# Performance work log

Hardware: AMD Instinct MI355X
Metric: run time of the kernel (lower is better)

## Reference

```python
import jax, jax.numpy as jnp
import numpy as np


def setup_inputs() -> dict:
    key = jax.random.key(0)
    k1, k2, k3, k4 = jax.random.split(key, 4)
    B, IN, OUT, R = 4096, 4096, 4096, 256
    x = jax.random.normal(k1, (B, IN), dtype=jnp.float32)
    U = jax.random.normal(k2, (R, IN), dtype=jnp.float32) / np.sqrt(IN)
    V = jax.random.normal(k3, (OUT, R), dtype=jnp.float32) / np.sqrt(R)
    bias = jax.random.uniform(k4, (OUT,), dtype=jnp.float32,
                              minval=-IN ** -0.5, maxval=IN ** -0.5)
    return {"x": x, "U": U, "V": V, "bias": bias}


def reference(x, U, V, bias):
    # Low-rank linear: out[b,j] = sum_k V[j,k] * (sum_i U[k,i] * x[b,i]) + bias[j]
    # (the torch loops with sparsity=1.0 / keep_stride==1 compute exactly this)
    t = jnp.einsum('bi,ri->br', x, U)        # [B, R]
    out = jnp.einsum('br,or->bo', t, V) + bias  # [B, OUT]
    return out
```

## Files before the change

### kernel.cpp

```cpp
#include <hip/hip_runtime.h>

typedef __attribute__((ext_vector_type(8))) short bf16x8;
typedef __attribute__((ext_vector_type(4))) float f32x4;

__device__ __forceinline__ unsigned short f2bf(float f) {
  unsigned int u = __float_as_uint(f);
  return (unsigned short)((u + 0x7fffu + ((u >> 16) & 1u)) >> 16);
}

__device__ __forceinline__ float bf2f(unsigned short s) {
  return __uint_as_float(((unsigned int)s) << 16);
}

__device__ __forceinline__ void gload_lds16(const void* g, void* l) {
  __builtin_amdgcn_global_load_lds((const __attribute__((address_space(1))) void*)g,
                                   (__attribute__((address_space(3))) void*)l,
                                   16, 0, 0);
}

__global__ void prep(const float* __restrict__ U, const float4* __restrict__ V,
                     unsigned short* __restrict__ Upk, ushort4* __restrict__ Vb) {
  int i = blockIdx.x * 256 + threadIdx.x;
  const int NUP = 128 * 16 * 64;
  if (i < NUP) {
    int l = i & 63, n = (i >> 6) & 15, jg = i >> 10;
    const float* src = U + (long long)(n * 16 + (l & 15)) * 4096 + jg * 32 + (l >> 4) * 8;
    float4 a = *(const float4*)src;
    float4 b = *(const float4*)(src + 4);
    ushort4 o0, o1;
    o0.x = f2bf(a.x); o0.y = f2bf(a.y); o0.z = f2bf(a.z); o0.w = f2bf(a.w);
    o1.x = f2bf(b.x); o1.y = f2bf(b.y); o1.z = f2bf(b.z); o1.w = f2bf(b.w);
    ushort4* d = (ushort4*)(Upk + (long long)i * 8);
    d[0] = o0; d[1] = o1;
  } else {
    int j = i - NUP;
    float4 v = V[j];
    ushort4 o;
    o.x = f2bf(v.x); o.y = f2bf(v.y); o.z = f2bf(v.z); o.w = f2bf(v.w);
    Vb[j] = o;
  }
}

__global__ __launch_bounds__(256, 1)
void gemm1_ures(const float* __restrict__ x, const unsigned short* __restrict__ Upk,
                unsigned short* __restrict__ P) {
  __shared__ unsigned short sU[8 * 16 * 64 * 8];

  const int tid = threadIdx.x;
  const int l = tid & 63;
  const int w = tid >> 6;
  const int mg = blockIdx.x;
  const int z  = blockIdx.z;
  const int lr = l & 15;
  const int lg = l >> 4;

  {
    const unsigned short* src = Upk + (long long)z * 65536;
#pragma unroll
    for (int is = 0; is < 32; ++is) {
      int eo = is * 2048 + tid * 8;
      gload_lds16(src + eo, &sU[eo]);
    }
  }

  const float* xbase = x + (long long)(mg * 256 + w * 16 + lr) * 4096 + z * 256 + lg * 8;

  float4 xr[2][8][2];
#define XLOAD(p, s)                                                     \
  {                                                                     \
    const float* px_ = xbase + (long long)(p) * 64 * 4096;              \
    _Pragma("unroll")                                                   \
    for (int j_ = 0; j_ < 8; ++j_) {                                    \
      xr[s][j_][0] = *(const float4*)(px_ + j_ * 32);                   \
      xr[s][j_][1] = *(const float4*)(px_ + j_ * 32 + 4);               \
    }                                                                   \
  }

  XLOAD(0, 0);
  __syncthreads();

  unsigned short* Pz = P + (long long)z * (4096LL * 256);

#pragma unroll
  for (int p = 0; p < 4; ++p) {
    if (p < 3) XLOAD(p + 1, (p + 1) & 1);
    f32x4 acc[16] = {};
#pragma unroll
    for (int j = 0; j < 8; ++j) {
      float4 u0 = xr[p & 1][j][0], u1 = xr[p & 1][j][1];
      bf16x8 af;
      af[0] = (short)f2bf(u0.x); af[1] = (short)f2bf(u0.y);
      af[2] = (short)f2bf(u0.z); af[3] = (short)f2bf(u0.w);
      af[4] = (short)f2bf(u1.x); af[5] = (short)f2bf(u1.y);
      af[6] = (short)f2bf(u1.z); af[7] = (short)f2bf(u1.w);
#pragma unroll
      for (int n = 0; n < 16; ++n) {
        bf16x8 bfr = *(const bf16x8*)&sU[((j * 16 + n) * 64 + l) * 8];
        acc[n] = __builtin_amdgcn_mfma_f32_16x16x32_bf16(af, bfr, acc[n], 0, 0, 0);
      }
    }
    const int r0 = mg * 256 + p * 64 + w * 16 + lg * 4;
#pragma unroll
    for (int n = 0; n < 16; ++n)
#pragma unroll
      for (int i2 = 0; i2 < 4; ++i2)
        Pz[(long long)(r0 + i2) * 256 + n * 16 + lr] = f2bf(acc[n][i2]);
  }
#undef XLOAD
}

__global__ void reduce16(const ushort4* __restrict__ P, ushort4* __restrict__ t) {
  const int S = 4096 * 256 / 4;
  int i = blockIdx.x * 256 + threadIdx.x;
  float sx = 0, sy = 0, sz = 0, sw = 0;
#pragma unroll
  for (int z = 0; z < 16; ++z) {
    ushort4 v = P[i + z * S];
    sx += bf2f(v.x); sy += bf2f(v.y); sz += bf2f(v.z); sw += bf2f(v.w);
  }
  ushort4 o;
  o.x = f2bf(sx); o.y = f2bf(sy); o.z = f2bf(sz); o.w = f2bf(sw);
  t[i] = o;
}

__global__ __launch_bounds__(256)
void gemm2(const unsigned short* __restrict__ A,
           const unsigned short* __restrict__ B,
           const float* __restrict__ bias,
           float* __restrict__ C) {
  constexpr int MREP = 4, NREP = 4;
  __shared__ unsigned short sA[2][128 * 32];
  __shared__ unsigned short sB[2][128 * 32];

  const int tid = threadIdx.x;
  const int l = tid & 63;
  const int w = tid >> 6;
  const int wm = (w >> 1) * 64;
  const int wn = (w & 1) * 64;
  const int rm = blockIdx.x * 128;
  const int rn = blockIdx.y * 128;
  const int lr = l & 15;
  const int lc8 = (l >> 4) * 8;

  auto stage = [&](int kt, int buf) {
    const int k0 = kt * 32;
#pragma unroll
    for (int is = 0; is < 2; ++is) {
      int eo = is * 2048 + tid * 8;
      gload_lds16(B + (long long)(rn + (eo >> 5)) * 256 + k0 + (eo & 31), &sB[buf][eo]);
    }
#pragma unroll
    for (int is = 0; is < 2; ++is) {
      int eo = is * 2048 + tid * 8;
      gload_lds16(A + (long long)(rm + (eo >> 5)) * 256 + k0 + (eo & 31), &sA[buf][eo]);
    }
  };

  f32x4 acc[MREP][NREP] = {};

  stage(0, 0);
  for (int kt = 0; kt < 8; ++kt) {
    __syncthreads();
    if (kt + 1 < 8) stage(kt + 1, (kt + 1) & 1);
    const unsigned short* a0 = sA[kt & 1];
    const unsigned short* b0 = sB[kt & 1];
    bf16x8 af[MREP], bfr[NREP];
#pragma unroll
    for (int m = 0; m < MREP; ++m)
      af[m] = *(const bf16x8*)&a0[(wm + m * 16 + lr) * 32 + lc8];
#pragma unroll
    for (int n = 0; n < NREP; ++n)
      bfr[n] = *(const bf16x8*)&b0[(wn + n * 16 + lr) * 32 + lc8];
#pragma unroll
    for (int m = 0; m < MREP; ++m)
#pragma unroll
      for (int n = 0; n < NREP; ++n)
        acc[m][n] = __builtin_amdgcn_mfma_f32_16x16x32_bf16(af[m], bfr[n], acc[m][n], 0, 0, 0);
  }

  const int r0 = rm + wm + (l >> 4) * 4;
  const int c0 = rn + wn + lr;
#pragma unroll
  for (int n = 0; n < NREP; ++n) {
    const int cc = c0 + n * 16;
    const float badd = bias[cc];
#pragma unroll
    for (int m = 0; m < MREP; ++m)
#pragma unroll
      for (int i = 0; i < 4; ++i)
        C[(long long)(r0 + m * 16 + i) * 4096 + cc] = acc[m][n][i] + badd;
  }
}

extern "C" void kernel_launch(void* const* d_in, const int* in_sizes, int n_in,
                              void* d_out, int out_size, void* d_ws, size_t ws_size,
                              hipStream_t stream) {
  const float* x    = (const float*)d_in[0];
  const float* U    = (const float*)d_in[1];
  const float* V    = (const float*)d_in[2];
  const float* bias = (const float*)d_in[3];
  float* out = (float*)d_out;

  char* ws = (char*)d_ws;
  unsigned short* P   = (unsigned short*)ws;
  unsigned short* tb  = (unsigned short*)(ws + (32u << 20));
  unsigned short* Upk = (unsigned short*)(ws + (34u << 20));
  unsigned short* Vb  = (unsigned short*)(ws + (36u << 20));

  prep<<<1536, 256, 0, stream>>>(U, (const float4*)V, Upk, (ushort4*)Vb);

  dim3 g1(16, 1, 16);
  gemm1_ures<<<g1, 256, 0, stream>>>(x, Upk, P);

  reduce16<<<(4096 * 256 / 4) / 256, 256, 0, stream>>>((const ushort4*)P, (ushort4*)tb);

  dim3 g2(32, 32, 1);
  gemm2<<<g2, 256, 0, stream>>>(tb, Vb, bias, out);
}
```

Before: 58.87 us.

## Restructure gemm1 to stage fp32 x and bf16 U tiles through swizzled LDS

Gemm1 no longer keeps the whole pre-packed U slice in LDS with x held in registers. It now uses a 64x256 output tile per block with double-buffered async global-to-LDS loads of fp32 x and row-major bf16 U. Both buffers are XOR-swizzled, and x is converted with the packed v_cvt_pk_bf16_f32 instruction. The U pre-pack kernel becomes a plain cast, and gemm2 gets the same LDS swizzle to reduce bank conflicts. The grid grows from 256 to 1024 blocks, trading the old register-resident x path for more occupancy and overlap.

```diff
diff --git a/kernel.cpp b/kernel.cpp
--- a/kernel.cpp
+++ b/kernel.cpp
@@ -10,6 +10,12 @@
 
 __device__ __forceinline__ float bf2f(unsigned short s) {
   return __uint_as_float(((unsigned int)s) << 16);
+}
+
+__device__ __forceinline__ unsigned int cvtpk(float a, float b) {
+  unsigned int w;
+  asm("v_cvt_pk_bf16_f32 %0, %1, %2" : "=v"(w) : "v"(a), "v"(b));
+  return w;
 }
 
 __device__ __forceinline__ void gload_lds16(const void* g, void* l) {
@@ -18,95 +24,95 @@
                                    16, 0, 0);
 }
 
-__global__ void prep(const float* __restrict__ U, const float4* __restrict__ V,
-                     unsigned short* __restrict__ Upk, ushort4* __restrict__ Vb) {
+__global__ void castUV(const float4* __restrict__ U, const float4* __restrict__ V,
+                       ushort4* __restrict__ Ub, ushort4* __restrict__ Vb) {
+  const int NU = 256 * 4096 / 4;
   int i = blockIdx.x * 256 + threadIdx.x;
-  const int NUP = 128 * 16 * 64;
-  if (i < NUP) {
-    int l = i & 63, n = (i >> 6) & 15, jg = i >> 10;
-    const float* src = U + (long long)(n * 16 + (l & 15)) * 4096 + jg * 32 + (l >> 4) * 8;
-    float4 a = *(const float4*)src;
-    float4 b = *(const float4*)(src + 4);
-    ushort4 o0, o1;
-    o0.x = f2bf(a.x); o0.y = f2bf(a.y); o0.z = f2bf(a.z); o0.w = f2bf(a.w);
-    o1.x = f2bf(b.x); o1.y = f2bf(b.y); o1.z = f2bf(b.z); o1.w = f2bf(b.w);
-    ushort4* d = (ushort4*)(Upk + (long long)i * 8);
-    d[0] = o0; d[1] = o1;
-  } else {
-    int j = i - NUP;
-    float4 v = V[j];
-    ushort4 o;
-    o.x = f2bf(v.x); o.y = f2bf(v.y); o.z = f2bf(v.z); o.w = f2bf(v.w);
-    Vb[j] = o;
-  }
-}
-
-__global__ __launch_bounds__(256, 1)
-void gemm1_ures(const float* __restrict__ x, const unsigned short* __restrict__ Upk,
+  const float4* s; ushort4* d; int j;
+  if (i < NU) { s = U; d = Ub; j = i; }
+  else        { s = V; d = Vb; j = i - NU; }
+  float4 v = s[j];
+  ushort4 o;
+  o.x = f2bf(v.x); o.y = f2bf(v.y); o.z = f2bf(v.z); o.w = f2bf(v.w);
+  d[j] = o;
+}
+
+__global__ __launch_bounds__(256)
+void gemm1_f32a(const float* __restrict__ x, const unsigned short* __restrict__ Ub,
                 unsigned short* __restrict__ P) {
-  __shared__ unsigned short sU[8 * 16 * 64 * 8];
+  __shared__ __align__(16) float sA[2][64 * 32];
+  __shared__ __align__(16) unsigned short sB[2][256 * 32];
 
   const int tid = threadIdx.x;
   const int l = tid & 63;
   const int w = tid >> 6;
-  const int mg = blockIdx.x;
-  const int z  = blockIdx.z;
+  const int wn = w * 64;
+  const int rm = blockIdx.x * 64;
+  const int k0base = blockIdx.z * 256;
   const int lr = l & 15;
   const int lg = l >> 4;
 
-  {
-    const unsigned short* src = Upk + (long long)z * 65536;
-#pragma unroll
-    for (int is = 0; is < 32; ++is) {
-      int eo = is * 2048 + tid * 8;
-      gload_lds16(src + eo, &sU[eo]);
-    }
-  }
-
-  const float* xbase = x + (long long)(mg * 256 + w * 16 + lr) * 4096 + z * 256 + lg * 8;
-
-  float4 xr[2][8][2];
-#define XLOAD(p, s)                                                     \
-  {                                                                     \
-    const float* px_ = xbase + (long long)(p) * 64 * 4096;              \
-    _Pragma("unroll")                                                   \
-    for (int j_ = 0; j_ < 8; ++j_) {                                    \
-      xr[s][j_][0] = *(const float4*)(px_ + j_ * 32);                   \
-      xr[s][j_][1] = *(const float4*)(px_ + j_ * 32 + 4);               \
-    }                                                                   \
-  }
-
-  XLOAD(0, 0);
-  __syncthreads();
-
-  unsigned short* Pz = P + (long long)z * (4096LL * 256);
-
-#pragma unroll
-  for (int p = 0; p < 4; ++p) {
-    if (p < 3) XLOAD(p + 1, (p + 1) & 1);
-    f32x4 acc[16] = {};
-#pragma unroll
-    for (int j = 0; j < 8; ++j) {
-      float4 u0 = xr[p & 1][j][0], u1 = xr[p & 1][j][1];
-      bf16x8 af;
-      af[0] = (short)f2bf(u0.x); af[1] = (short)f2bf(u0.y);
-      af[2] = (short)f2bf(u0.z); af[3] = (short)f2bf(u0.w);
-      af[4] = (short)f2bf(u1.x); af[5] = (short)f2bf(u1.y);
-      af[6] = (short)f2bf(u1.z); af[7] = (short)f2bf(u1.w);
-#pragma unroll
-      for (int n = 0; n < 16; ++n) {
-        bf16x8 bfr = *(const bf16x8*)&sU[((j * 16 + n) * 64 + l) * 8];
-        acc[n] = __builtin_amdgcn_mfma_f32_16x16x32_bf16(af, bfr, acc[n], 0, 0, 0);
-      }
-    }
-    const int r0 = mg * 256 + p * 64 + w * 16 + lg * 4;
-#pragma unroll
-    for (int n = 0; n < 16; ++n)
-#pragma unroll
-      for (int i2 = 0; i2 < 4; ++i2)
-        Pz[(long long)(r0 + i2) * 256 + n * 16 + lr] = f2bf(acc[n][i2]);
-  }
-#undef XLOAD
+  auto stage = [&](int kt, int buf) {
+    const int k0 = k0base + kt * 32;
+#pragma unroll
+    for (int is = 0; is < 4; ++is) {
+      int s = is * 256 + tid;
+      int r = s >> 2;
+      gload_lds16(Ub + (long long)r * 4096 + k0 + 8 * ((s & 3) ^ (r & 3)),
+                  (char*)sB[buf] + s * 16);
+    }
+#pragma unroll
+    for (int is = 0; is < 2; ++is) {
+      int s = is * 256 + tid;
+      int r = s >> 3;
+      gload_lds16(x + (long long)(rm + r) * 4096 + k0 + 4 * ((s & 7) ^ (r & 7)),
+                  (char*)sA[buf] + s * 16);
+    }
+  };
+
+  f32x4 acc[4][4] = {};
+
+  stage(0, 0);
+  for (int kt = 0; kt < 8; ++kt) {
+    __syncthreads();
+    if (kt < 7) stage(kt + 1, (kt + 1) & 1);
+    const char* a0 = (const char*)sA[kt & 1];
+    const char* b0 = (const char*)sB[kt & 1];
+    bf16x8 af[4], bfr[4];
+#pragma unroll
+    for (int m = 0; m < 4; ++m) {
+      const int row = m * 16 + lr;
+      const int byte0 = row * 128 + ((lg * 32) ^ ((row & 7) << 4));
+      float4 f0 = *(const float4*)(a0 + byte0);
+      float4 f1 = *(const float4*)(a0 + (byte0 ^ 16));
+      unsigned int w0 = cvtpk(f0.x, f0.y), w1 = cvtpk(f0.z, f0.w);
+      unsigned int w2 = cvtpk(f1.x, f1.y), w3 = cvtpk(f1.z, f1.w);
+      uint4 packed = {w0, w1, w2, w3};
+      af[m] = __builtin_bit_cast(bf16x8, packed);
+    }
+#pragma unroll
+    for (int n = 0; n < 4; ++n) {
+      const int row = wn + n * 16 + lr;
+      bfr[n] = *(const bf16x8*)(b0 + row * 64 + ((lg * 16) ^ ((row & 3) << 4)));
+    }
+#pragma unroll
+    for (int m = 0; m < 4; ++m)
+#pragma unroll
+      for (int n = 0; n < 4; ++n)
+        acc[m][n] = __builtin_amdgcn_mfma_f32_16x16x32_bf16(af[m], bfr[n], acc[m][n], 0, 0, 0);
+  }
+
+  unsigned short* Pz = P + (long long)blockIdx.z * (4096LL * 256);
+  const int r0 = rm + lg * 4;
+#pragma unroll
+  for (int n = 0; n < 4; ++n) {
+    const int cc = wn + n * 16 + lr;
+#pragma unroll
+    for (int m = 0; m < 4; ++m)
+#pragma unroll
+      for (int i = 0; i < 4; ++i)
+        Pz[(long long)(r0 + m * 16 + i) * 256 + cc] = f2bf(acc[m][n][i]);
+  }
 }
 
 __global__ void reduce16(const ushort4* __restrict__ P, ushort4* __restrict__ t) {
@@ -128,9 +134,8 @@
            const unsigned short* __restrict__ B,
            const float* __restrict__ bias,
            float* __restrict__ C) {
-  constexpr int MREP = 4, NREP = 4;
-  __shared__ unsigned short sA[2][128 * 32];
-  __shared__ unsigned short sB[2][128 * 32];
+  __shared__ __align__(16) unsigned short sA[2][128 * 32];
+  __shared__ __align__(16) unsigned short sB[2][128 * 32];
 
   const int tid = threadIdx.x;
   const int l = tid & 63;
@@ -140,52 +145,60 @@
   const int rm = blockIdx.x * 128;
   const int rn = blockIdx.y * 128;
   const int lr = l & 15;
-  const int lc8 = (l >> 4) * 8;
+  const int lg = l >> 4;
 
   auto stage = [&](int kt, int buf) {
     const int k0 = kt * 32;
 #pragma unroll
     for (int is = 0; is < 2; ++is) {
-      int eo = is * 2048 + tid * 8;
-      gload_lds16(B + (long long)(rn + (eo >> 5)) * 256 + k0 + (eo & 31), &sB[buf][eo]);
+      int s = is * 256 + tid;
+      int r = s >> 2;
+      gload_lds16(B + (long long)(rn + r) * 256 + k0 + 8 * ((s & 3) ^ (r & 3)),
+                  (char*)sB[buf] + s * 16);
     }
 #pragma unroll
     for (int is = 0; is < 2; ++is) {
-      int eo = is * 2048 + tid * 8;
-      gload_lds16(A + (long long)(rm + (eo >> 5)) * 256 + k0 + (eo & 31), &sA[buf][eo]);
+      int s = is * 256 + tid;
+      int r = s >> 2;
+      gload_lds16(A + (long long)(rm + r) * 256 + k0 + 8 * ((s & 3) ^ (r & 3)),
+                  (char*)sA[buf] + s * 16);
     }
   };
 
-  f32x4 acc[MREP][NREP] = {};
+  f32x4 acc[4][4] = {};
 
   stage(0, 0);
   for (int kt = 0; kt < 8; ++kt) {
     __syncthreads();
-    if (kt + 1 < 8) stage(kt + 1, (kt + 1) & 1);
-    const unsigned short* a0 = sA[kt & 1];
-    const unsigned short* b0 = sB[kt & 1];
-    bf16x8 af[MREP], bfr[NREP];
-#pragma unroll
-    for (int m = 0; m < MREP; ++m)
-      af[m] = *(const bf16x8*)&a0[(wm + m * 16 + lr) * 32 + lc8];
-#pragma unroll
-    for (int n = 0; n < NREP; ++n)
-      bfr[n] = *(const bf16x8*)&b0[(wn + n * 16 + lr) * 32 + lc8];
-#pragma unroll
-    for (int m = 0; m < MREP; ++m)
-#pragma unroll
-      for (int n = 0; n < NREP; ++n)
+    if (kt < 7) stage(kt + 1, (kt + 1) & 1);
+    const char* a0 = (const char*)sA[kt & 1];
+    const char* b0 = (const char*)sB[kt & 1];
+    bf16x8 af[4], bfr[4];
+#pragma unroll
+    for (int m = 0; m < 4; ++m) {
+      const int row = wm + m * 16 + lr;
+      af[m] = *(const bf16x8*)(a0 + row * 64 + ((lg * 16) ^ ((row & 3) << 4)));
+    }
+#pragma unroll
+    for (int n = 0; n < 4; ++n) {
+      const int row = wn + n * 16 + lr;
+      bfr[n] = *(const bf16x8*)(b0 + row * 64 + ((lg * 16) ^ ((row & 3) << 4)));
+    }
+#pragma unroll
+    for (int m = 0; m < 4; ++m)
+#pragma unroll
+      for (int n = 0; n < 4; ++n)
         acc[m][n] = __builtin_amdgcn_mfma_f32_16x16x32_bf16(af[m], bfr[n], acc[m][n], 0, 0, 0);
   }
 
-  const int r0 = rm + wm + (l >> 4) * 4;
+  const int r0 = rm + wm + lg * 4;
   const int c0 = rn + wn + lr;
 #pragma unroll
-  for (int n = 0; n < NREP; ++n) {
+  for (int n = 0; n < 4; ++n) {
     const int cc = c0 + n * 16;
     const float badd = bias[cc];
 #pragma unroll
-    for (int m = 0; m < MREP; ++m)
+    for (int m = 0; m < 4; ++m)
 #pragma unroll
       for (int i = 0; i < 4; ++i)
         C[(long long)(r0 + m * 16 + i) * 4096 + cc] = acc[m][n][i] + badd;
@@ -204,15 +217,16 @@
   char* ws = (char*)d_ws;
   unsigned short* P   = (unsigned short*)ws;
   unsigned short* tb  = (unsigned short*)(ws + (32u << 20));
-  unsigned short* Upk = (unsigned short*)(ws + (34u << 20));
+  unsigned short* Ub  = (unsigned short*)(ws + (34u << 20));
   unsigned short* Vb  = (unsigned short*)(ws + (36u << 20));
 
-  prep<<<1536, 256, 0, stream>>>(U, (const float4*)V, Upk, (ushort4*)Vb);
-
-  dim3 g1(16, 1, 16);
-  gemm1_ures<<<g1, 256, 0, stream>>>(x, Upk, P);
-
-  reduce16<<<(4096 * 256 / 4) / 256, 256, 0, stream>>>((const ushort4*)P, (ushort4*)tb);
+  castUV<<<2048, 256, 0, stream>>>((const float4*)U, (const float4*)V,
+                                   (ushort4*)Ub, (ushort4*)Vb);
+
+  dim3 g1(64, 1, 16);
+  gemm1_f32a<<<g1, 256, 0, stream>>>(x, Ub, P);
+
+  reduce16<<<1024, 256, 0, stream>>>((const ushort4*)P, (ushort4*)tb);
 
   dim3 g2(32, 32, 1);
   gemm2<<<g2, 256, 0, stream>>>(tb, Vb, bias, out);
```

New measurement: 63.82 us. 1.08x slower.
